# Performance work log

Hardware: AMD Instinct MI355X
Metric: run time of the kernel (lower is better)

## Reference

```python
import jax, jax.numpy as jnp
import numpy as np


def setup_inputs() -> dict:
    key = jax.random.key(0)
    ks = jax.random.split(key, 16)
    B, P, N, E = 16, 12, 20000, 320000
    f32 = jnp.float32
    x = jax.random.normal(ks[0], (B, P, N), f32)
    input_mask = (jax.random.uniform(ks[1], (B, P, N)) > 0.2).astype(f32)  # GAIN observed mask
    noise = jax.random.uniform(ks[2], (B, P, N), f32) * 0.01  # Uniform(0, 0.01) noise matrix
    edge_index = jax.random.randint(ks[3], (2, E), 0, N)
    edge_weights = jax.random.uniform(ks[4], (E,), f32)

    def lin(k, fi, fo):
        return jax.random.normal(k, (fi, fo), f32) * (1.0 / np.sqrt(fi))

    params = dict(
        Wz=lin(ks[5], 2, P), bz=jnp.zeros((P,), f32),
        Wr=lin(ks[6], 2, P), br=jnp.zeros((P,), f32),
        Wh=lin(ks[7], 2, P), bh=jnp.zeros((P,), f32),
        Lz_w=lin(ks[8], 2 * P, P), Lz_b=jnp.zeros((P,), f32),
        Lr_w=lin(ks[9], 2 * P, P), Lr_b=jnp.zeros((P,), f32),
        Lh_w=lin(ks[10], 2 * P, P), Lh_b=jnp.zeros((P,), f32),
        attention=jax.random.uniform(ks[11], (P,), f32),
        W1=lin(ks[12], P, P), b1=jnp.zeros((P,), f32),
        W2=lin(ks[13], P, P), b2=jnp.zeros((P,), f32),
    )
    return dict(x=x, input_mask=input_mask, noise=noise,
                edge_index=edge_index, edge_weights=edge_weights, **params)


def reference(x, input_mask, noise, edge_index, edge_weights,
              Wz, bz, Wr, br, Wh, bh,
              Lz_w, Lz_b, Lr_w, Lr_b, Lh_w, Lh_b,
              attention, W1, b1, W2, b2):
    B, P, N = x.shape
    # GAIN: fill missing entries with small uniform noise
    x = input_mask * x + (1.0 - input_mask) * noise
    # stack([x, mask]) -> [2,B,P,N]; permute(1,3,0,2) -> [B,N,2,P]; we scan over periods
    X = jnp.transpose(jnp.stack([x, input_mask], axis=2), (1, 0, 3, 2))  # [P, B, N, 2]

    # GCNConv symmetric normalization with self-loops (fill_value = 1)
    src, dst = edge_index[0], edge_index[1]
    loop = jnp.arange(N)
    src_sl = jnp.concatenate([src, loop])
    dst_sl = jnp.concatenate([dst, loop])
    w_sl = jnp.concatenate([edge_weights, jnp.ones((N,), x.dtype)])
    deg = jnp.zeros((N,), x.dtype).at[dst_sl].add(w_sl)
    dinv = jnp.where(deg > 0, deg ** -0.5, 0.0)
    norm = dinv[src_sl] * w_sl * dinv[dst_sl]  # [E + N]

    probs = jax.nn.softmax(attention)  # attention over periods
    H0 = jnp.zeros((B, N, P), x.dtype)  # A3TGCN2 never updates H -> each period sees H = 0

    def step(acc, inp):
        Xt, p = inp  # Xt: [B, N, 2]
        # aggregate raw 2-dim features then apply the (linear) GCN weight: same math,
        # far cheaper than gathering the projected [B, E, P] messages
        msgs = Xt[:, src_sl, :] * norm[None, :, None]          # [B, E+N, 2]
        agg = jnp.zeros_like(Xt).at[:, dst_sl, :].add(msgs)    # [B, N, 2]
        xz = agg @ Wz + bz
        xr = agg @ Wr + br
        xh = agg @ Wh + bh
        Z = jax.nn.sigmoid(jnp.concatenate([xz, H0], axis=-1) @ Lz_w + Lz_b)
        R = jax.nn.sigmoid(jnp.concatenate([xr, H0], axis=-1) @ Lr_w + Lr_b)
        Ht = jnp.tanh(jnp.concatenate([xh, H0 * R], axis=-1) @ Lh_w + Lh_b)
        H = Z * H0 + (1.0 - Z) * Ht
        return acc + p * H, None

    H_accum, _ = jax.lax.scan(step, H0, (X, probs))  # [B, N, P]

    # MLP head: ReLU -> Linear -> ReLU -> Linear -> Sigmoid
    h = jax.nn.relu(H_accum)
    h = jax.nn.relu(h @ W1 + b1)
    imput = jax.nn.sigmoid(h @ W2 + b2)               # [B, N, P]
    imputation = jnp.transpose(imput, (0, 2, 1))      # [B, P, N]
    res = input_mask * x + (1.0 - input_mask) * imputation
    return res, imputation
```

## Files before the change

kernel.cpp:

```cpp
#include <hip/hip_runtime.h>

#define NN 20000
#define NE 320000
#define BB 16
#define PP 12
#define NCOL 384
#define OUT_OFF (BB*PP*NN)

__device__ __forceinline__ float sigmoidf_(float v) {
    return __fdividef(1.f, 1.f + __expf(-v));
}
__device__ __forceinline__ float tanh_fast(float v) {
    v = fminf(fmaxf(v, -15.f), 15.f);
    float e = __expf(-2.f * v);
    return __fdividef(1.f - e, 1.f + e);
}

__global__ __launch_bounds__(256) void init_kernel(float* deg, int* cnt) {
    int i = blockIdx.x * 256 + threadIdx.x;
    if (i < NN) { deg[i] = 1.0f; cnt[i] = 0; }
}

__global__ __launch_bounds__(256) void degcnt_kernel(const int* __restrict__ ei,
                                                     const float* __restrict__ ew,
                                                     float* deg, int* cnt) {
    int e = blockIdx.x * 256 + threadIdx.x;
    if (e < NE) {
        int d = ei[NE + e];
        atomicAdd(&deg[d], ew[e]);
        atomicAdd(&cnt[d], 1);
    }
}

__global__ __launch_bounds__(256) void dinv_kernel(const float* __restrict__ deg,
                                                   float* __restrict__ dinv) {
    int i = blockIdx.x * 256 + threadIdx.x;
    if (i < NN) {
        float dg = deg[i];
        dinv[i] = dg > 0.f ? 1.0f / sqrtf(dg) : 0.f;
    }
}

__global__ __launch_bounds__(1024) void scan_kernel(const int* __restrict__ cnt,
                                                    int* __restrict__ rowp,
                                                    int* __restrict__ cur) {
    __shared__ int lds[1024];
    int tid = threadIdx.x;
    int base = 0;
    for (int start = 0; start < NN; start += 1024) {
        int i = start + tid;
        int v = (i < NN) ? cnt[i] : 0;
        lds[tid] = v;
        __syncthreads();
        for (int off = 1; off < 1024; off <<= 1) {
            int add = (tid >= off) ? lds[tid - off] : 0;
            __syncthreads();
            lds[tid] += add;
            __syncthreads();
        }
        int incl = lds[tid];
        int total = lds[1023];
        if (i < NN) { int ex = base + incl - v; rowp[i] = ex; cur[i] = ex; }
        base += total;
        __syncthreads();
    }
    if (tid == 0) rowp[NN] = base;
}

__global__ __launch_bounds__(256) void scatter_kernel(const int* __restrict__ ei,
                                                      const float* __restrict__ ew,
                                                      const float* __restrict__ dinv,
                                                      int* cur, int* __restrict__ ecol,
                                                      float* __restrict__ eval) {
    int e = blockIdx.x * 256 + threadIdx.x;
    if (e < NE) {
        int s = ei[e];
        int d = ei[NE + e];
        int pos = atomicAdd(&cur[d], 1);
        ecol[pos] = s;
        eval[pos] = dinv[s] * ew[e] * dinv[d];
    }
}

__global__ __launch_bounds__(256) void prep_kernel(const float* __restrict__ Wz, const float* __restrict__ bz,
                                                   const float* __restrict__ Wh, const float* __restrict__ bh,
                                                   const float* __restrict__ Lzw, const float* __restrict__ Lzb,
                                                   const float* __restrict__ Lhw, const float* __restrict__ Lhb,
                                                   const float* __restrict__ att,
                                                   const float* __restrict__ W1, const float* __restrict__ b1,
                                                   const float* __restrict__ W2, const float* __restrict__ b2,
                                                   float* __restrict__ cst) {
    int t = threadIdx.x;
    if (t < PP) {
        int p = t;
        float az0 = 0.f, az1 = 0.f, cz = 0.f, ah0 = 0.f, ah1 = 0.f, ch = 0.f;
        for (int q = 0; q < PP; ++q) {
            float lz = Lzw[q * PP + p], lh = Lhw[q * PP + p];
            az0 += Wz[q] * lz;
            az1 += Wz[PP + q] * lz;
            cz  += bz[q] * lz;
            ah0 += Wh[q] * lh;
            ah1 += Wh[PP + q] * lh;
            ch  += bh[q] * lh;
        }
        cz += Lzb[p]; ch += Lhb[p];
        cst[p] = az0; cst[12 + p] = az1; cst[24 + p] = cz;
        cst[36 + p] = ah0; cst[48 + p] = ah1; cst[60 + p] = ch;
        float m = att[0];
        for (int q = 1; q < PP; ++q) m = fmaxf(m, att[q]);
        float ssum = 0.f;
        for (int q = 0; q < PP; ++q) ssum += __expf(att[q] - m);
        cst[72 + p] = __expf(att[p] - m) / ssum;
    }
    if (t < 144) { cst[84 + t] = W1[t]; cst[240 + t] = W2[t]; }
    if (t < PP) { cst[228 + t] = b1[t]; cst[384 + t] = b2[t]; }
}

#define TILE 32
__global__ __launch_bounds__(256) void buildx_kernel(const float* __restrict__ x,
                                                     const float* __restrict__ mask,
                                                     const float* __restrict__ noise,
                                                     float* __restrict__ X) {
    __shared__ float tile[TILE][NCOL + 1];
    int tid = threadIdx.x;
    int n0 = blockIdx.x * TILE;
    int i = tid & 31;
    int prb = tid >> 5;
    #pragma unroll 4
    for (int it = 0; it < 24; ++it) {
        int pr = it * 8 + prb;
        int g = pr * NN + n0 + i;
        float m = mask[g];
        float xv = x[g];
        float nz = noise[g];
        float xf = m * xv + (1.f - m) * nz;
        int col = pr * 2;
        tile[i][col]     = xf;
        tile[i][col + 1] = m;
    }
    __syncthreads();
    #pragma unroll 4
    for (int it = 0; it < 48; ++it) {
        int idx = it * 256 + tid;
        int r = idx / NCOL;
        int c = idx - r * NCOL;
        X[(n0 + r) * NCOL + c] = tile[r][c];
    }
}

__global__ __launch_bounds__(256) void spmm_kernel(const float* __restrict__ X,
                                                   const float* __restrict__ dinv,
                                                   const int* __restrict__ rowp,
                                                   const int* __restrict__ ecol,
                                                   const float* __restrict__ eval,
                                                   float* __restrict__ agg) {
    int wave = threadIdx.x >> 6;
    int lane = threadIdx.x & 63;
    int d = __builtin_amdgcn_readfirstlane(blockIdx.x * 4 + wave);
    int r0 = rowp[d];
    int r1 = rowp[d + 1];
    float di = dinv[d];
    float acc[6];
    const float* xr = X + d * NCOL + lane;
    #pragma unroll
    for (int k = 0; k < 6; ++k) acc[k] = di * di * xr[k * 64];
    for (int e = r0; e < r1; ++e) {
        int s = ecol[e];
        float v = eval[e];
        const float* xs = X + s * NCOL + lane;
        #pragma unroll
        for (int k = 0; k < 6; ++k) acc[k] += v * xs[k * 64];
    }
    float* ag = agg + d * NCOL + lane;
    #pragma unroll
    for (int k = 0; k < 6; ++k) ag[k * 64] = acc[k];
}

__global__ __launch_bounds__(256) void pointwise_kernel(const float* __restrict__ agg,
                                                        const float* __restrict__ cst,
                                                        const float* __restrict__ x,
                                                        const float* __restrict__ mask,
                                                        float* __restrict__ out) {
    __shared__ float C[396];
    int tid = threadIdx.x;
    for (int i = tid; i < 396; i += 256) C[i] = cst[i];
    __syncthreads();
    int idx = blockIdx.x * 256 + tid;
    int b = idx / NN;
    int n = idx - b * NN;
    float A[24];
    const float4* ap = (const float4*)(agg + (size_t)n * NCOL + b * 24);
    #pragma unroll
    for (int k = 0; k < 6; ++k) {
        float4 v = ap[k];
        A[4 * k + 0] = v.x; A[4 * k + 1] = v.y; A[4 * k + 2] = v.z; A[4 * k + 3] = v.w;
    }
    float h1[12];
    #pragma unroll
    for (int p = 0; p < 12; ++p) {
        float az0 = C[p], az1 = C[12 + p], czp = C[24 + p];
        float ah0 = C[36 + p], ah1 = C[48 + p], chp = C[60 + p];
        float hp = 0.f;
        #pragma unroll
        for (int t = 0; t < 12; ++t) {
            float a0 = A[2 * t], a1 = A[2 * t + 1];
            float z  = sigmoidf_(a0 * az0 + a1 * az1 + czp);
            float th = tanh_fast(a0 * ah0 + a1 * ah1 + chp);
            hp += C[72 + t] * ((1.f - z) * th);
        }
        h1[p] = fmaxf(hp, 0.f);
    }
    float h2[12];
    #pragma unroll
    for (int p = 0; p < 12; ++p) {
        float s = C[228 + p];
        #pragma unroll
        for (int q = 0; q < 12; ++q) s += h1[q] * C[84 + q * 12 + p];
        h2[p] = fmaxf(s, 0.f);
    }
    #pragma unroll
    for (int p = 0; p < 12; ++p) {
        float s = C[384 + p];
        #pragma unroll
        for (int q = 0; q < 12; ++q) s += h2[q] * C[240 + q * 12 + p];
        float imp = sigmoidf_(s);
        int o = (b * PP + p) * NN + n;
        float m = mask[o];
        float xv = x[o];
        out[o] = m * xv + (1.f - m) * imp;
        out[OUT_OFF + o] = imp;
    }
}

extern "C" void kernel_launch(void* const* d_in, const int* in_sizes, int n_in,
                              void* d_out, int out_size, void* d_ws, size_t ws_size,
                              hipStream_t stream) {
    const float* x     = (const float*)d_in[0];
    const float* mask  = (const float*)d_in[1];
    const float* noise = (const float*)d_in[2];
    const int*   ei    = (const int*)d_in[3];
    const float* ew    = (const float*)d_in[4];
    const float* Wz    = (const float*)d_in[5];
    const float* bz    = (const float*)d_in[6];
    const float* Wh    = (const float*)d_in[9];
    const float* bh    = (const float*)d_in[10];
    const float* Lzw   = (const float*)d_in[11];
    const float* Lzb   = (const float*)d_in[12];
    const float* Lhw   = (const float*)d_in[15];
    const float* Lhb   = (const float*)d_in[16];
    const float* att   = (const float*)d_in[17];
    const float* W1    = (const float*)d_in[18];
    const float* b1    = (const float*)d_in[19];
    const float* W2    = (const float*)d_in[20];
    const float* b2    = (const float*)d_in[21];
    float* out = (float*)d_out;

    float* Xf   = (float*)d_ws;
    float* AGG  = Xf + (size_t)NN * NCOL;
    float* DEG  = AGG + (size_t)NN * NCOL;
    float* DINV = DEG + NN;
    float* EVAL = DINV + NN;
    float* CST  = EVAL + NE;
    int*   CNT  = (int*)(CST + 512);
    int*   ROWP = CNT + NN;
    int*   CUR  = ROWP + NN + 1;
    int*   ECOL = CUR + NN;

    hipLaunchKernelGGL(init_kernel,    dim3((NN + 255) / 256), dim3(256), 0, stream, DEG, CNT);
    hipLaunchKernelGGL(degcnt_kernel,  dim3((NE + 255) / 256), dim3(256), 0, stream, ei, ew, DEG, CNT);
    hipLaunchKernelGGL(dinv_kernel,    dim3((NN + 255) / 256), dim3(256), 0, stream, DEG, DINV);
    hipLaunchKernelGGL(scan_kernel,    dim3(1), dim3(1024), 0, stream, CNT, ROWP, CUR);
    hipLaunchKernelGGL(scatter_kernel, dim3((NE + 255) / 256), dim3(256), 0, stream, ei, ew, DINV, CUR, ECOL, EVAL);
    hipLaunchKernelGGL(prep_kernel,    dim3(1), dim3(256), 0, stream,
                       Wz, bz, Wh, bh, Lzw, Lzb, Lhw, Lhb, att, W1, b1, W2, b2, CST);
    hipLaunchKernelGGL(buildx_kernel,  dim3(NN / TILE), dim3(256), 0, stream, x, mask, noise, Xf);
    hipLaunchKernelGGL(spmm_kernel,    dim3(NN / 4), dim3(256), 0, stream, Xf, DINV, ROWP, ECOL, EVAL, AGG);
    hipLaunchKernelGGL(pointwise_kernel, dim3((BB * NN) / 256), dim3(256), 0, stream, AGG, CST, x, mask, out);
}
```

Baseline: 362.6 us.

## Split SpMM columns into slices, pack edge data, and fuse dinv into scan

The SpMM now assigns each wave a 48-column slice of a destination row instead of all 384 columns. This gives eight times more blocks so more gathers are in flight, and the edge loop is unrolled by four. Edge column and weight are packed into one int2 array and read with nontemporal loads. The scan kernel becomes a per-thread serial block scan plus a single LDS pass instead of 20 sequential passes, and it also computes dinv, which removes one launch. In exchange, a quarter of the lanes sit idle in the SpMM and each slice reloads the same edge list.

```diff
diff --git a/kernel.cpp b/kernel.cpp
--- a/kernel.cpp
+++ b/kernel.cpp
@@ -6,6 +6,8 @@
 #define PP 12
 #define NCOL 384
 #define OUT_OFF (BB*PP*NN)
+#define SLICES 8
+#define SCOLS 48
 
 __device__ __forceinline__ float sigmoidf_(float v) {
     return __fdividef(1.f, 1.f + __expf(-v));
@@ -32,53 +34,56 @@
     }
 }
 
-__global__ __launch_bounds__(256) void dinv_kernel(const float* __restrict__ deg,
-                                                   float* __restrict__ dinv) {
-    int i = blockIdx.x * 256 + threadIdx.x;
-    if (i < NN) {
-        float dg = deg[i];
-        dinv[i] = dg > 0.f ? 1.0f / sqrtf(dg) : 0.f;
-    }
-}
-
 __global__ __launch_bounds__(1024) void scan_kernel(const int* __restrict__ cnt,
+                                                    const float* __restrict__ deg,
                                                     int* __restrict__ rowp,
-                                                    int* __restrict__ cur) {
+                                                    int* __restrict__ cur,
+                                                    float* __restrict__ dinv) {
     __shared__ int lds[1024];
     int tid = threadIdx.x;
-    int base = 0;
-    for (int start = 0; start < NN; start += 1024) {
-        int i = start + tid;
+    int base = tid * 20;
+    int local[20];
+    int s = 0;
+    #pragma unroll
+    for (int k = 0; k < 20; ++k) {
+        int i = base + k;
         int v = (i < NN) ? cnt[i] : 0;
-        lds[tid] = v;
+        local[k] = s;
+        s += v;
+    }
+    lds[tid] = s;
+    __syncthreads();
+    for (int off = 1; off < 1024; off <<= 1) {
+        int add = (tid >= off) ? lds[tid - off] : 0;
         __syncthreads();
-        for (int off = 1; off < 1024; off <<= 1) {
-            int add = (tid >= off) ? lds[tid - off] : 0;
-            __syncthreads();
-            lds[tid] += add;
-            __syncthreads();
-        }
-        int incl = lds[tid];
-        int total = lds[1023];
-        if (i < NN) { int ex = base + incl - v; rowp[i] = ex; cur[i] = ex; }
-        base += total;
+        lds[tid] += add;
         __syncthreads();
     }
-    if (tid == 0) rowp[NN] = base;
+    int pre = (tid > 0) ? lds[tid - 1] : 0;
+    #pragma unroll
+    for (int k = 0; k < 20; ++k) {
+        int i = base + k;
+        if (i < NN) {
+            int ex = pre + local[k];
+            rowp[i] = ex; cur[i] = ex;
+            float dg = deg[i];
+            dinv[i] = dg > 0.f ? 1.0f / sqrtf(dg) : 0.f;
+        }
+    }
+    if (tid == 0) rowp[NN] = lds[1023];
 }
 
 __global__ __launch_bounds__(256) void scatter_kernel(const int* __restrict__ ei,
                                                       const float* __restrict__ ew,
                                                       const float* __restrict__ dinv,
-                                                      int* cur, int* __restrict__ ecol,
-                                                      float* __restrict__ eval) {
+                                                      int* cur, int2* __restrict__ epk) {
     int e = blockIdx.x * 256 + threadIdx.x;
     if (e < NE) {
         int s = ei[e];
         int d = ei[NE + e];
         int pos = atomicAdd(&cur[d], 1);
-        ecol[pos] = s;
-        eval[pos] = dinv[s] * ew[e] * dinv[d];
+        float v = dinv[s] * ew[e] * dinv[d];
+        epk[pos] = make_int2(s, __float_as_int(v));
     }
 }
 
@@ -151,29 +156,45 @@
 __global__ __launch_bounds__(256) void spmm_kernel(const float* __restrict__ X,
                                                    const float* __restrict__ dinv,
                                                    const int* __restrict__ rowp,
-                                                   const int* __restrict__ ecol,
-                                                   const float* __restrict__ eval,
+                                                   const int2* __restrict__ epk,
                                                    float* __restrict__ agg) {
+    int slice = blockIdx.x & 7;
+    int grp   = blockIdx.x >> 3;
     int wave = threadIdx.x >> 6;
     int lane = threadIdx.x & 63;
-    int d = __builtin_amdgcn_readfirstlane(blockIdx.x * 4 + wave);
+    int d = __builtin_amdgcn_readfirstlane(grp * 4 + wave);
+    int c = slice * SCOLS + lane;
+    bool act = lane < SCOLS;
+    float di = dinv[d];
+    float acc = 0.f;
+    if (act) acc = di * di * X[(size_t)d * NCOL + c];
     int r0 = rowp[d];
     int r1 = rowp[d + 1];
-    float di = dinv[d];
-    float acc[6];
-    const float* xr = X + d * NCOL + lane;
-    #pragma unroll
-    for (int k = 0; k < 6; ++k) acc[k] = di * di * xr[k * 64];
-    for (int e = r0; e < r1; ++e) {
-        int s = ecol[e];
-        float v = eval[e];
-        const float* xs = X + s * NCOL + lane;
-        #pragma unroll
-        for (int k = 0; k < 6; ++k) acc[k] += v * xs[k * 64];
-    }
-    float* ag = agg + d * NCOL + lane;
-    #pragma unroll
-    for (int k = 0; k < 6; ++k) ag[k * 64] = acc[k];
+    const long long* ep = (const long long*)epk;
+    int e = r0;
+    for (; e + 4 <= r1; e += 4) {
+        long long p0 = __builtin_nontemporal_load(ep + e);
+        long long p1 = __builtin_nontemporal_load(ep + e + 1);
+        long long p2 = __builtin_nontemporal_load(ep + e + 2);
+        long long p3 = __builtin_nontemporal_load(ep + e + 3);
+        int s0 = (int)p0; float v0 = __int_as_float((int)(p0 >> 32));
+        int s1 = (int)p1; float v1 = __int_as_float((int)(p1 >> 32));
+        int s2 = (int)p2; float v2 = __int_as_float((int)(p2 >> 32));
+        int s3 = (int)p3; float v3 = __int_as_float((int)(p3 >> 32));
+        if (act) {
+            float x0 = X[(size_t)s0 * NCOL + c];
+            float x1 = X[(size_t)s1 * NCOL + c];
+            float x2 = X[(size_t)s2 * NCOL + c];
+            float x3 = X[(size_t)s3 * NCOL + c];
+            acc += v0 * x0; acc += v1 * x1; acc += v2 * x2; acc += v3 * x3;
+        }
+    }
+    for (; e < r1; ++e) {
+        long long p0 = __builtin_nontemporal_load(ep + e);
+        int s0 = (int)p0; float v0 = __int_as_float((int)(p0 >> 32));
+        if (act) acc += v0 * X[(size_t)s0 * NCOL + c];
+    }
+    if (act) __builtin_nontemporal_store(acc, &agg[(size_t)d * NCOL + c]);
 }
 
 __global__ __launch_bounds__(256) void pointwise_kernel(const float* __restrict__ agg,
@@ -257,23 +278,21 @@
 
     float* Xf   = (float*)d_ws;
     float* AGG  = Xf + (size_t)NN * NCOL;
-    float* DEG  = AGG + (size_t)NN * NCOL;
+    int2*  EPK  = (int2*)(AGG + (size_t)NN * NCOL);
+    float* DEG  = (float*)(EPK + NE);
     float* DINV = DEG + NN;
-    float* EVAL = DINV + NN;
-    float* CST  = EVAL + NE;
+    float* CST  = DINV + NN;
     int*   CNT  = (int*)(CST + 512);
     int*   ROWP = CNT + NN;
     int*   CUR  = ROWP + NN + 1;
-    int*   ECOL = CUR + NN;
 
     hipLaunchKernelGGL(init_kernel,    dim3((NN + 255) / 256), dim3(256), 0, stream, DEG, CNT);
     hipLaunchKernelGGL(degcnt_kernel,  dim3((NE + 255) / 256), dim3(256), 0, stream, ei, ew, DEG, CNT);
-    hipLaunchKernelGGL(dinv_kernel,    dim3((NN + 255) / 256), dim3(256), 0, stream, DEG, DINV);
-    hipLaunchKernelGGL(scan_kernel,    dim3(1), dim3(1024), 0, stream, CNT, ROWP, CUR);
-    hipLaunchKernelGGL(scatter_kernel, dim3((NE + 255) / 256), dim3(256), 0, stream, ei, ew, DINV, CUR, ECOL, EVAL);
+    hipLaunchKernelGGL(scan_kernel,    dim3(1), dim3(1024), 0, stream, CNT, DEG, ROWP, CUR, DINV);
+    hipLaunchKernelGGL(scatter_kernel, dim3((NE + 255) / 256), dim3(256), 0, stream, ei, ew, DINV, CUR, EPK);
     hipLaunchKernelGGL(prep_kernel,    dim3(1), dim3(256), 0, stream,
                        Wz, bz, Wh, bh, Lzw, Lzb, Lhw, Lhb, att, W1, b1, W2, b2, CST);
     hipLaunchKernelGGL(buildx_kernel,  dim3(NN / TILE), dim3(256), 0, stream, x, mask, noise, Xf);
-    hipLaunchKernelGGL(spmm_kernel,    dim3(NN / 4), dim3(256), 0, stream, Xf, DINV, ROWP, ECOL, EVAL, AGG);
+    hipLaunchKernelGGL(spmm_kernel,    dim3(SLICES * NN / 4), dim3(256), 0, stream, Xf, DINV, ROWP, EPK, AGG);
     hipLaunchKernelGGL(pointwise_kernel, dim3((BB * NN) / 256), dim3(256), 0, stream, AGG, CST, x, mask, out);
 }
```

Result: slower. 378.8 us (+4.4%).
